# Kernel tuning notes

Hardware: AMD Instinct MI355X
Metric: run time of the kernel (lower is better)

## Reference

```python
import jax, jax.numpy as jnp
import numpy as np

SEQ_LEN = 256
SPIKE_STEPS = 7
BATCH = 128
IN_DIM = 96
HIDDEN = 512
OUT_DIM = 2
NLAYERS = 3
ALPHA = 2.0  # atan surrogate alpha = 2 * grad_slope


@jax.custom_vjp
def spike(x):
    # Heaviside fire with snntorch ATan surrogate gradient.
    return (x > 0).astype(x.dtype)


def _spike_fwd(x):
    return (x > 0).astype(x.dtype), x


def _spike_bwd(x, g):
    return (g * (ALPHA / 2.0) / (1.0 + (jnp.pi / 2.0 * ALPHA * x) ** 2),)


spike.defvjp(_spike_fwd, _spike_bwd)


def setup_inputs() -> dict:
    key = jax.random.key(0)
    ks = jax.random.split(key, 5)
    x = jax.random.normal(ks[0], (SEQ_LEN, BATCH, IN_DIM), dtype=jnp.float32)
    def w(k, shape, fan_in):
        return jax.random.normal(k, shape, dtype=jnp.float32) / np.float32(np.sqrt(fan_in))
    W0 = w(ks[1], (HIDDEN, IN_DIM), IN_DIM)
    W1 = w(ks[2], (HIDDEN, HIDDEN), HIDDEN)
    W2 = w(ks[3], (HIDDEN, HIDDEN), HIDDEN)
    Wout = w(ks[4], (OUT_DIM, HIDDEN), HIDDEN)
    betas = jnp.full((NLAYERS,), 0.95, dtype=jnp.float32)  # learnable beta per LIF layer
    thrs = jnp.ones((NLAYERS,), dtype=jnp.float32)          # learnable threshold per LIF layer
    return dict(x=x, W0=W0, W1=W1, W2=W2, Wout=Wout, betas=betas, thrs=thrs)


def reference(x, W0, W1, W2, Wout, betas, thrs):
    """Seq2SeqSNN forward (eval mode: dropout is identity).

    Membrane / integrator state is reset only once at the start (i == 0 path
    of the torch forward), so the whole seq_len * spike_steps loop is a single
    recurrence of length T = SEQ_LEN * SPIKE_STEPS.
    LIF layer (snntorch Leaky, reset_mechanism='zero'):
        reset = stop_grad(heaviside(mem_prev - thr))
        mem   = (beta * mem_prev + cur) * (1 - reset)
        spk   = spike(mem - thr)
    Output layer (Integrator, reset 'none'): mem_out += Wout @ z; the decoded
    prediction per sequence step is the mean of mem_out over spike_steps.
    """
    Ws = (W0, W1, W2)
    x_rep = jnp.repeat(x, SPIKE_STEPS, axis=0)  # [T, B, F], same input for each inner spike step

    mems0 = tuple(jnp.zeros((BATCH, HIDDEN), dtype=x.dtype) for _ in range(NLAYERS))
    mem_out0 = jnp.zeros((BATCH, OUT_DIM), dtype=x.dtype)

    def step(carry, xt):
        mems, mem_out = carry
        z = xt
        new_mems = []
        for j in range(NLAYERS):
            cur = z @ Ws[j].T                                   # [B, H]
            reset = jax.lax.stop_gradient(spike(mems[j] - thrs[j]))
            mem = (betas[j] * mems[j] + cur) * (1.0 - reset)
            z = spike(mem - thrs[j])                            # binary spikes
            new_mems.append(mem)
        mem_out = mem_out + z @ Wout.T                           # integrator, no reset
        return (tuple(new_mems), mem_out), mem_out

    _, mem_out_seq = jax.lax.scan(step, (mems0, mem_out0), x_rep)  # [T, B, 2]
    # decoder='mean' over the spike_steps axis of each sequence step
    preds = mem_out_seq.reshape(SEQ_LEN, SPIKE_STEPS, BATCH, OUT_DIM).mean(axis=1)
    return preds  # [SEQ_LEN, BATCH, OUT_DIM]
```

## Files before the change

### kernel.cpp

```cpp
#include <hip/hip_runtime.h>

#define SEQ_LEN 256
#define SPIKE_STEPS 7
#define BATCH 128
#define IN_DIM 96
#define HIDDEN 512
#define OUT_DIM 2

#define W0T_OFF 0
#define W1T_OFF (IN_DIM * HIDDEN)
#define W2T_OFF (W1T_OFF + HIDDEN * HIDDEN)
#define CTR_BYTE_OFF ((size_t)(W2T_OFF + HIDDEN * HIDDEN) * sizeof(float))
#define ZBUF_BYTE_OFF (CTR_BYTE_OFF + 1024)

typedef float f32x4 __attribute__((ext_vector_type(4)));
typedef float f32x2 __attribute__((ext_vector_type(2)));

__global__ void transpose_kernel(const float* __restrict__ in, float* __restrict__ out,
                                 int rows, int cols) {
    int idx = blockIdx.x * blockDim.x + threadIdx.x;
    if (idx < rows * cols) {
        int r = idx / cols, c = idx - r * cols;
        out[c * rows + r] = in[idx];
    }
}

__device__ __forceinline__ void pkfma(f32x2& acc, float w, f32x2 m) {
    const f32x2 wv = {w, w};
    acc = __builtin_elementwise_fma(wv, m, acc);
}

__device__ __forceinline__ void union_sum7(const float* __restrict__ W,
                                           const int* __restrict__ act,
                                           const float (* __restrict__ fmp)[8],
                                           int npad, int tid,
                                           f32x2* __restrict__ acc) {
    if (npad <= 0) return;
    const float* Wt = W + tid;
    int rows[16];
    float wc[16];
    {
        const int4* av = reinterpret_cast<const int4*>(act);
        int4 a0 = av[0], a1 = av[1], a2 = av[2], a3 = av[3];
        rows[0]=a0.x; rows[1]=a0.y; rows[2]=a0.z; rows[3]=a0.w;
        rows[4]=a1.x; rows[5]=a1.y; rows[6]=a1.z; rows[7]=a1.w;
        rows[8]=a2.x; rows[9]=a2.y; rows[10]=a2.z; rows[11]=a2.w;
        rows[12]=a3.x; rows[13]=a3.y; rows[14]=a3.z; rows[15]=a3.w;
    }
    #pragma unroll
    for (int k = 0; k < 16; ++k) wc[k] = Wt[rows[k] * HIDDEN];

    for (int n = 16; n < npad; n += 16) {
        int nrows[16];
        float wn[16];
        {
            const int4* av = reinterpret_cast<const int4*>(act + n);
            int4 a0 = av[0], a1 = av[1], a2 = av[2], a3 = av[3];
            nrows[0]=a0.x; nrows[1]=a0.y; nrows[2]=a0.z; nrows[3]=a0.w;
            nrows[4]=a1.x; nrows[5]=a1.y; nrows[6]=a1.z; nrows[7]=a1.w;
            nrows[8]=a2.x; nrows[9]=a2.y; nrows[10]=a2.z; nrows[11]=a2.w;
            nrows[12]=a3.x; nrows[13]=a3.y; nrows[14]=a3.z; nrows[15]=a3.w;
        }
        #pragma unroll
        for (int k = 0; k < 16; ++k) wn[k] = Wt[nrows[k] * HIDDEN];

        const int base = n - 16;
        #pragma unroll
        for (int k = 0; k < 16; ++k) {
            f32x4 fa = *reinterpret_cast<const f32x4*>(&fmp[base + k][0]);
            f32x4 fb = *reinterpret_cast<const f32x4*>(&fmp[base + k][4]);
            pkfma(acc[0], wc[k], __builtin_shufflevector(fa, fa, 0, 1));
            pkfma(acc[1], wc[k], __builtin_shufflevector(fa, fa, 2, 3));
            pkfma(acc[2], wc[k], __builtin_shufflevector(fb, fb, 0, 1));
            pkfma(acc[3], wc[k], __builtin_shufflevector(fb, fb, 2, 3));
        }
        #pragma unroll
        for (int k = 0; k < 16; ++k) wc[k] = wn[k];
    }
    const int base = npad - 16;
    #pragma unroll
    for (int k = 0; k < 16; ++k) {
        f32x4 fa = *reinterpret_cast<const f32x4*>(&fmp[base + k][0]);
        f32x4 fb = *reinterpret_cast<const f32x4*>(&fmp[base + k][4]);
        pkfma(acc[0], wc[k], __builtin_shufflevector(fa, fa, 0, 1));
        pkfma(acc[1], wc[k], __builtin_shufflevector(fa, fa, 2, 3));
        pkfma(acc[2], wc[k], __builtin_shufflevector(fb, fb, 0, 1));
        pkfma(acc[3], wc[k], __builtin_shufflevector(fb, fb, 2, 3));
    }
}

__device__ __forceinline__ int build_union(const unsigned long long (*zm7)[8],
                                           int* act, float (*fmp)[8],
                                           int wid, int lane, int tid, int m7) {
    unsigned long long um[8];
    #pragma unroll
    for (int q = 0; q < 8; ++q) {
        unsigned long long u = zm7[0][q];
        #pragma unroll
        for (int s = 1; s < SPIKE_STEPS; ++s) u |= zm7[s][q];
        um[q] = u;
    }
    int pre = 0, total = 0;
    #pragma unroll
    for (int q = 0; q < 8; ++q) {
        int p = __popcll(um[q]);
        total += p;
        if (q < wid) pre += p;
    }
    if (m7 != 0) {
        int rank = pre + __popcll(um[wid] & ((1ull << lane) - 1ull));
        act[rank] = tid;
        f32x4 v0, v4;
        #pragma unroll
        for (int s = 0; s < 4; ++s) v0[s] = ((m7 >> s) & 1) ? 1.0f : 0.0f;
        #pragma unroll
        for (int s = 0; s < 3; ++s) v4[s] = ((m7 >> (4 + s)) & 1) ? 1.0f : 0.0f;
        v4[3] = 0.f;
        *reinterpret_cast<f32x4*>(&fmp[rank][0]) = v0;
        *reinterpret_cast<f32x4*>(&fmp[rank][4]) = v4;
    }
    int npad = (total + 15) & ~15;
    if (tid < npad - total) {
        act[total + tid] = 0;
        const f32x4 z = {0.f, 0.f, 0.f, 0.f};
        *reinterpret_cast<f32x4*>(&fmp[total + tid][0]) = z;
        *reinterpret_cast<f32x4*>(&fmp[total + tid][4]) = z;
    }
    return npad;
}

__launch_bounds__(512, 1)
__global__ void snn_pipe_kernel(const float* __restrict__ x,
                                const float* __restrict__ Wout,
                                const float* __restrict__ betas,
                                const float* __restrict__ thrs,
                                const float* __restrict__ W0T,
                                const float* __restrict__ W1T,
                                const float* __restrict__ W2T,
                                unsigned long long* __restrict__ zbuf,
                                int* __restrict__ ctr,
                                float* __restrict__ out)
{
    const int b    = blockIdx.x >> 1;
    const int role = blockIdx.x & 1;
    const int tid  = threadIdx.x;
    const int lane = tid & 63;
    const int wid  = tid >> 6;

    __shared__ float xs[2][IN_DIM];
    __shared__ unsigned long long zm7[SPIKE_STEPS][8];
    __shared__ int act[HIDDEN];
    __shared__ __align__(16) float fmp[HIDDEN][8];
    __shared__ float red[16];

    if (role == 0) {
        const float beta0 = betas[0], beta1 = betas[1];
        const float thr0  = thrs[0],  thr1  = thrs[1];
        float mem0 = 0.f, mem1 = 0.f;
        unsigned long long* zb = zbuf + (size_t)b * SEQ_LEN * 56;

        if (tid < IN_DIM) xs[0][tid] = x[(0 * BATCH + b) * IN_DIM + tid];
        __syncthreads();

        for (int i = 0; i < SEQ_LEN; ++i) {
            const int cur = i & 1;

            float cur0 = 0.f;
            #pragma unroll 8
            for (int k = 0; k < IN_DIM; ++k)
                cur0 = __fmaf_rn(xs[cur][k], W0T[k * HIDDEN + tid], cur0);

            if (i + 1 < SEQ_LEN && tid < IN_DIM)
                xs[cur ^ 1][tid] = x[((i + 1) * BATCH + b) * IN_DIM + tid];

            int m7 = 0;
            #pragma unroll
            for (int s = 0; s < SPIKE_STEPS; ++s) {
                bool reset0 = (mem0 - thr0) > 0.f;
                mem0 = reset0 ? 0.f : __fadd_rn(__fmul_rn(beta0, mem0), cur0);
                bool z0 = (mem0 - thr0) > 0.f;
                m7 |= (int)z0 << s;
                unsigned long long bal = __ballot(z0);
                if (lane == 0) zm7[s][wid] = bal;
            }
            __syncthreads();

            int npad = build_union(zm7, act, fmp, wid, lane, tid, m7);
            __syncthreads();

            f32x2 acc[4] = {{0.f,0.f},{0.f,0.f},{0.f,0.f},{0.f,0.f}};
            union_sum7(W1T, act, fmp, npad, tid, acc);
            const float accs[SPIKE_STEPS] =
                {acc[0].x, acc[0].y, acc[1].x, acc[1].y, acc[2].x, acc[2].y, acc[3].x};

            #pragma unroll
            for (int s = 0; s < SPIKE_STEPS; ++s) {
                bool reset1 = (mem1 - thr1) > 0.f;
                mem1 = reset1 ? 0.f : __fadd_rn(__fmul_rn(beta1, mem1), accs[s]);
                bool z1 = (mem1 - thr1) > 0.f;
                unsigned long long bal1 = __ballot(z1);
                if (lane == 0)
                    __hip_atomic_store(&zb[(size_t)i * 56 + s * 8 + wid], bal1,
                                       __ATOMIC_RELAXED, __HIP_MEMORY_SCOPE_AGENT);
            }
            __syncthreads();
            if (tid == 0)
                __hip_atomic_store(&ctr[b], i + 1,
                                   __ATOMIC_RELAXED, __HIP_MEMORY_SCOPE_AGENT);
        }
    } else {
        const float beta2 = betas[2];
        const float thr2  = thrs[2];
        const float wo0 = Wout[tid];
        const float wo1 = Wout[HIDDEN + tid];
        float mem2 = 0.f;
        float a0s = 0.f, a1s = 0.f;
        const unsigned long long* zb = zbuf + (size_t)b * SEQ_LEN * 56;

        for (int i = 0; i < SEQ_LEN; ++i) {
            if (tid < 56) {
                while (__hip_atomic_load(&ctr[b], __ATOMIC_RELAXED,
                                         __HIP_MEMORY_SCOPE_AGENT) < i + 1)
                    __builtin_amdgcn_s_sleep(1);
                ((unsigned long long*)zm7)[tid] =
                    __hip_atomic_load(&zb[(size_t)i * 56 + tid],
                                      __ATOMIC_RELAXED, __HIP_MEMORY_SCOPE_AGENT);
            }
            __syncthreads();

            int m7 = 0;
            #pragma unroll
            for (int s = 0; s < SPIKE_STEPS; ++s)
                m7 |= (int)((zm7[s][wid] >> lane) & 1ull) << s;

            int npad = build_union(zm7, act, fmp, wid, lane, tid, m7);
            __syncthreads();

            f32x2 acc[4] = {{0.f,0.f},{0.f,0.f},{0.f,0.f},{0.f,0.f}};
            union_sum7(W2T, act, fmp, npad, tid, acc);
            const float accs[SPIKE_STEPS] =
                {acc[0].x, acc[0].y, acc[1].x, acc[1].y, acc[2].x, acc[2].y, acc[3].x};

            float w0 = 0.f, w1 = 0.f;
            #pragma unroll
            for (int s = 0; s < SPIKE_STEPS; ++s) {
                bool reset2 = (mem2 - thr2) > 0.f;
                mem2 = reset2 ? 0.f : __fadd_rn(__fmul_rn(beta2, mem2), accs[s]);
                bool z2 = (mem2 - thr2) > 0.f;
                a0s += z2 ? wo0 : 0.f;
                a1s += z2 ? wo1 : 0.f;
                w0 += a0s;
                w1 += a1s;
            }

            float r0 = w0, r1 = w1;
            #pragma unroll
            for (int off = 32; off > 0; off >>= 1) {
                r0 += __shfl_down(r0, off);
                r1 += __shfl_down(r1, off);
            }
            if (lane == 0) { red[wid * 2] = r0; red[wid * 2 + 1] = r1; }
            __syncthreads();
            if (tid == 0) {
                float s0 = 0.f, s1 = 0.f;
                #pragma unroll
                for (int q = 0; q < 8; ++q) { s0 += red[q * 2]; s1 += red[q * 2 + 1]; }
                out[(i * BATCH + b) * OUT_DIM + 0] = s0 / 7.0f;
                out[(i * BATCH + b) * OUT_DIM + 1] = s1 / 7.0f;
            }
        }
    }
}

extern "C" void kernel_launch(void* const* d_in, const int* in_sizes, int n_in,
                              void* d_out, int out_size, void* d_ws, size_t ws_size,
                              hipStream_t stream) {
    const float* x     = (const float*)d_in[0];
    const float* W0    = (const float*)d_in[1];
    const float* W1    = (const float*)d_in[2];
    const float* W2    = (const float*)d_in[3];
    const float* Wout  = (const float*)d_in[4];
    const float* betas = (const float*)d_in[5];
    const float* thrs  = (const float*)d_in[6];
    float* out = (float*)d_out;

    float* ws  = (float*)d_ws;
    float* W0T = ws + W0T_OFF;
    float* W1T = ws + W1T_OFF;
    float* W2T = ws + W2T_OFF;
    int* ctr = (int*)((char*)d_ws + CTR_BYTE_OFF);
    unsigned long long* zbuf = (unsigned long long*)((char*)d_ws + ZBUF_BYTE_OFF);

    {
        int n = HIDDEN * IN_DIM;
        transpose_kernel<<<(n + 255) / 256, 256, 0, stream>>>(W0, W0T, HIDDEN, IN_DIM);
    }
    {
        int n = HIDDEN * HIDDEN;
        transpose_kernel<<<(n + 255) / 256, 256, 0, stream>>>(W1, W1T, HIDDEN, HIDDEN);
        transpose_kernel<<<(n + 255) / 256, 256, 0, stream>>>(W2, W2T, HIDDEN, HIDDEN);
    }

    hipMemsetAsync((char*)d_ws + CTR_BYTE_OFF, 0, 1024, stream);

    snn_pipe_kernel<<<2 * BATCH, HIDDEN, 0, stream>>>(
        x, Wout, betas, thrs, W0T, W1T, W2T, zbuf, ctr, out);
}
```

Measured before the change: 2.946 ms.

## Merge producer/consumer blocks into one 1024-thread block with LDS handoff

Replaces the two-block-per-batch pipeline, which handed layer-1 spikes to layer 2 through global memory and an atomic counter spin-wait, with a single 1024-thread block per batch element. The first half computes layers 0-1 while the second half computes layer 2 for the previous step, exchanging spike masks through double-buffered shared memory and block barriers. This removes global-memory polling latency and the memset, but couples both halves to the same barriers, so each step waits for the slower half, and it doubles LDS usage per block.

```diff
diff --git a/kernel.cpp b/kernel.cpp
--- a/kernel.cpp
+++ b/kernel.cpp
@@ -10,8 +10,6 @@
 #define W0T_OFF 0
 #define W1T_OFF (IN_DIM * HIDDEN)
 #define W2T_OFF (W1T_OFF + HIDDEN * HIDDEN)
-#define CTR_BYTE_OFF ((size_t)(W2T_OFF + HIDDEN * HIDDEN) * sizeof(float))
-#define ZBUF_BYTE_OFF (CTR_BYTE_OFF + 1024)
 
 typedef float f32x4 __attribute__((ext_vector_type(4)));
 typedef float f32x2 __attribute__((ext_vector_type(2)));
@@ -33,10 +31,10 @@
 __device__ __forceinline__ void union_sum7(const float* __restrict__ W,
                                            const int* __restrict__ act,
                                            const float (* __restrict__ fmp)[8],
-                                           int npad, int tid,
+                                           int npad, int col,
                                            f32x2* __restrict__ acc) {
     if (npad <= 0) return;
-    const float* Wt = W + tid;
+    const float* Wt = W + col;
     int rows[16];
     float wc[16];
     {
@@ -89,15 +87,15 @@
     }
 }
 
-__device__ __forceinline__ int build_union(const unsigned long long (*zm7)[8],
+__device__ __forceinline__ int build_union(const unsigned long long (*zm)[8],
                                            int* act, float (*fmp)[8],
-                                           int wid, int lane, int tid, int m7) {
+                                           int hwid, int hlane, int htid, int m7) {
     unsigned long long um[8];
     #pragma unroll
     for (int q = 0; q < 8; ++q) {
-        unsigned long long u = zm7[0][q];
-        #pragma unroll
-        for (int s = 1; s < SPIKE_STEPS; ++s) u |= zm7[s][q];
+        unsigned long long u = zm[0][q];
+        #pragma unroll
+        for (int s = 1; s < SPIKE_STEPS; ++s) u |= zm[s][q];
         um[q] = u;
     }
     int pre = 0, total = 0;
@@ -105,11 +103,11 @@
     for (int q = 0; q < 8; ++q) {
         int p = __popcll(um[q]);
         total += p;
-        if (q < wid) pre += p;
+        if (q < hwid) pre += p;
     }
     if (m7 != 0) {
-        int rank = pre + __popcll(um[wid] & ((1ull << lane) - 1ull));
-        act[rank] = tid;
+        int rank = pre + __popcll(um[hwid] & ((1ull << hlane) - 1ull));
+        act[rank] = htid;
         f32x4 v0, v4;
         #pragma unroll
         for (int s = 0; s < 4; ++s) v0[s] = ((m7 >> s) & 1) ? 1.0f : 0.0f;
@@ -120,60 +118,65 @@
         *reinterpret_cast<f32x4*>(&fmp[rank][4]) = v4;
     }
     int npad = (total + 15) & ~15;
-    if (tid < npad - total) {
-        act[total + tid] = 0;
+    if (htid < npad - total) {
+        act[total + htid] = 0;
         const f32x4 z = {0.f, 0.f, 0.f, 0.f};
-        *reinterpret_cast<f32x4*>(&fmp[total + tid][0]) = z;
-        *reinterpret_cast<f32x4*>(&fmp[total + tid][4]) = z;
+        *reinterpret_cast<f32x4*>(&fmp[total + htid][0]) = z;
+        *reinterpret_cast<f32x4*>(&fmp[total + htid][4]) = z;
     }
     return npad;
 }
 
-__launch_bounds__(512, 1)
-__global__ void snn_pipe_kernel(const float* __restrict__ x,
-                                const float* __restrict__ Wout,
-                                const float* __restrict__ betas,
-                                const float* __restrict__ thrs,
-                                const float* __restrict__ W0T,
-                                const float* __restrict__ W1T,
-                                const float* __restrict__ W2T,
-                                unsigned long long* __restrict__ zbuf,
-                                int* __restrict__ ctr,
-                                float* __restrict__ out)
+__launch_bounds__(1024, 1)
+__global__ void snn_merged_kernel(const float* __restrict__ x,
+                                  const float* __restrict__ Wout,
+                                  const float* __restrict__ betas,
+                                  const float* __restrict__ thrs,
+                                  const float* __restrict__ W0T,
+                                  const float* __restrict__ W1T,
+                                  const float* __restrict__ W2T,
+                                  float* __restrict__ out)
 {
-    const int b    = blockIdx.x >> 1;
-    const int role = blockIdx.x & 1;
-    const int tid  = threadIdx.x;
-    const int lane = tid & 63;
-    const int wid  = tid >> 6;
+    const int b     = blockIdx.x;
+    const int tid   = threadIdx.x;
+    const int half  = tid >> 9;
+    const int htid  = tid & 511;
+    const int hlane = htid & 63;
+    const int hwid  = htid >> 6;
 
     __shared__ float xs[2][IN_DIM];
-    __shared__ unsigned long long zm7[SPIKE_STEPS][8];
-    __shared__ int act[HIDDEN];
-    __shared__ __align__(16) float fmp[HIDDEN][8];
+    __shared__ unsigned long long zm0[SPIKE_STEPS][8];
+    __shared__ unsigned long long zr[2][SPIKE_STEPS][8];
+    __shared__ int actF[HIDDEN];
+    __shared__ int actB[HIDDEN];
+    __shared__ __align__(16) float fmpF[HIDDEN][8];
+    __shared__ __align__(16) float fmpB[HIDDEN][8];
     __shared__ float red[16];
 
-    if (role == 0) {
-        const float beta0 = betas[0], beta1 = betas[1];
-        const float thr0  = thrs[0],  thr1  = thrs[1];
-        float mem0 = 0.f, mem1 = 0.f;
-        unsigned long long* zb = zbuf + (size_t)b * SEQ_LEN * 56;
-
-        if (tid < IN_DIM) xs[0][tid] = x[(0 * BATCH + b) * IN_DIM + tid];
-        __syncthreads();
-
-        for (int i = 0; i < SEQ_LEN; ++i) {
-            const int cur = i & 1;
-
+    float mem0 = 0.f, mem1 = 0.f;
+    float mem2 = 0.f, a0s = 0.f, a1s = 0.f;
+    const float beta0 = betas[0], beta1 = betas[1], beta2 = betas[2];
+    const float thr0  = thrs[0],  thr1  = thrs[1],  thr2  = thrs[2];
+    const float wo0 = Wout[htid];
+    const float wo1 = Wout[HIDDEN + htid];
+
+    if (half == 0 && tid < IN_DIM) xs[0][tid] = x[(0 * BATCH + b) * IN_DIM + tid];
+    __syncthreads();
+
+    for (int it = 0; it <= SEQ_LEN; ++it) {
+        const bool frun = (half == 0) && (it < SEQ_LEN);
+        const bool brun = (half == 1) && (it >= 1);
+
+        int m7 = 0;
+        if (frun) {
+            const int cur = it & 1;
             float cur0 = 0.f;
             #pragma unroll 8
             for (int k = 0; k < IN_DIM; ++k)
-                cur0 = __fmaf_rn(xs[cur][k], W0T[k * HIDDEN + tid], cur0);
-
-            if (i + 1 < SEQ_LEN && tid < IN_DIM)
-                xs[cur ^ 1][tid] = x[((i + 1) * BATCH + b) * IN_DIM + tid];
-
-            int m7 = 0;
+                cur0 = __fmaf_rn(xs[cur][k], W0T[k * HIDDEN + htid], cur0);
+            if (it + 1 < SEQ_LEN && htid < IN_DIM)
+                xs[cur ^ 1][htid] = x[((it + 1) * BATCH + b) * IN_DIM + htid];
+
             #pragma unroll
             for (int s = 0; s < SPIKE_STEPS; ++s) {
                 bool reset0 = (mem0 - thr0) > 0.f;
@@ -181,66 +184,39 @@
                 bool z0 = (mem0 - thr0) > 0.f;
                 m7 |= (int)z0 << s;
                 unsigned long long bal = __ballot(z0);
-                if (lane == 0) zm7[s][wid] = bal;
-            }
-            __syncthreads();
-
-            int npad = build_union(zm7, act, fmp, wid, lane, tid, m7);
-            __syncthreads();
-
+                if (hlane == 0) zm0[s][hwid] = bal;
+            }
+        } else if (brun) {
+            const unsigned long long (*zs)[8] = zr[(it - 1) & 1];
+            #pragma unroll
+            for (int s = 0; s < SPIKE_STEPS; ++s)
+                m7 |= (int)((zs[s][hwid] >> hlane) & 1ull) << s;
+        }
+        __syncthreads();
+
+        int npad = 0;
+        if (frun)      npad = build_union(zm0,              actF, fmpF, hwid, hlane, htid, m7);
+        else if (brun) npad = build_union(zr[(it - 1) & 1], actB, fmpB, hwid, hlane, htid, m7);
+        __syncthreads();
+
+        if (frun) {
             f32x2 acc[4] = {{0.f,0.f},{0.f,0.f},{0.f,0.f},{0.f,0.f}};
-            union_sum7(W1T, act, fmp, npad, tid, acc);
+            union_sum7(W1T, actF, fmpF, npad, htid, acc);
             const float accs[SPIKE_STEPS] =
                 {acc[0].x, acc[0].y, acc[1].x, acc[1].y, acc[2].x, acc[2].y, acc[3].x};
-
             #pragma unroll
             for (int s = 0; s < SPIKE_STEPS; ++s) {
                 bool reset1 = (mem1 - thr1) > 0.f;
                 mem1 = reset1 ? 0.f : __fadd_rn(__fmul_rn(beta1, mem1), accs[s]);
                 bool z1 = (mem1 - thr1) > 0.f;
                 unsigned long long bal1 = __ballot(z1);
-                if (lane == 0)
-                    __hip_atomic_store(&zb[(size_t)i * 56 + s * 8 + wid], bal1,
-                                       __ATOMIC_RELAXED, __HIP_MEMORY_SCOPE_AGENT);
-            }
-            __syncthreads();
-            if (tid == 0)
-                __hip_atomic_store(&ctr[b], i + 1,
-                                   __ATOMIC_RELAXED, __HIP_MEMORY_SCOPE_AGENT);
-        }
-    } else {
-        const float beta2 = betas[2];
-        const float thr2  = thrs[2];
-        const float wo0 = Wout[tid];
-        const float wo1 = Wout[HIDDEN + tid];
-        float mem2 = 0.f;
-        float a0s = 0.f, a1s = 0.f;
-        const unsigned long long* zb = zbuf + (size_t)b * SEQ_LEN * 56;
-
-        for (int i = 0; i < SEQ_LEN; ++i) {
-            if (tid < 56) {
-                while (__hip_atomic_load(&ctr[b], __ATOMIC_RELAXED,
-                                         __HIP_MEMORY_SCOPE_AGENT) < i + 1)
-                    __builtin_amdgcn_s_sleep(1);
-                ((unsigned long long*)zm7)[tid] =
-                    __hip_atomic_load(&zb[(size_t)i * 56 + tid],
-                                      __ATOMIC_RELAXED, __HIP_MEMORY_SCOPE_AGENT);
-            }
-            __syncthreads();
-
-            int m7 = 0;
-            #pragma unroll
-            for (int s = 0; s < SPIKE_STEPS; ++s)
-                m7 |= (int)((zm7[s][wid] >> lane) & 1ull) << s;
-
-            int npad = build_union(zm7, act, fmp, wid, lane, tid, m7);
-            __syncthreads();
-
+                if (hlane == 0) zr[it & 1][s][hwid] = bal1;
+            }
+        } else if (brun) {
             f32x2 acc[4] = {{0.f,0.f},{0.f,0.f},{0.f,0.f},{0.f,0.f}};
-            union_sum7(W2T, act, fmp, npad, tid, acc);
+            union_sum7(W2T, actB, fmpB, npad, htid, acc);
             const float accs[SPIKE_STEPS] =
                 {acc[0].x, acc[0].y, acc[1].x, acc[1].y, acc[2].x, acc[2].y, acc[3].x};
-
             float w0 = 0.f, w1 = 0.f;
             #pragma unroll
             for (int s = 0; s < SPIKE_STEPS; ++s) {
@@ -252,22 +228,22 @@
                 w0 += a0s;
                 w1 += a1s;
             }
-
             float r0 = w0, r1 = w1;
             #pragma unroll
             for (int off = 32; off > 0; off >>= 1) {
                 r0 += __shfl_down(r0, off);
                 r1 += __shfl_down(r1, off);
             }
-            if (lane == 0) { red[wid * 2] = r0; red[wid * 2 + 1] = r1; }
-            __syncthreads();
-            if (tid == 0) {
-                float s0 = 0.f, s1 = 0.f;
-                #pragma unroll
-                for (int q = 0; q < 8; ++q) { s0 += red[q * 2]; s1 += red[q * 2 + 1]; }
-                out[(i * BATCH + b) * OUT_DIM + 0] = s0 / 7.0f;
-                out[(i * BATCH + b) * OUT_DIM + 1] = s1 / 7.0f;
-            }
+            if (hlane == 0) { red[hwid * 2] = r0; red[hwid * 2 + 1] = r1; }
+        }
+        __syncthreads();
+
+        if (brun && htid == 0) {
+            float s0 = 0.f, s1 = 0.f;
+            #pragma unroll
+            for (int q = 0; q < 8; ++q) { s0 += red[q * 2]; s1 += red[q * 2 + 1]; }
+            out[((it - 1) * BATCH + b) * OUT_DIM + 0] = s0 / 7.0f;
+            out[((it - 1) * BATCH + b) * OUT_DIM + 1] = s1 / 7.0f;
         }
     }
 }
@@ -288,8 +264,6 @@
     float* W0T = ws + W0T_OFF;
     float* W1T = ws + W1T_OFF;
     float* W2T = ws + W2T_OFF;
-    int* ctr = (int*)((char*)d_ws + CTR_BYTE_OFF);
-    unsigned long long* zbuf = (unsigned long long*)((char*)d_ws + ZBUF_BYTE_OFF);
 
     {
         int n = HIDDEN * IN_DIM;
@@ -301,8 +275,6 @@
         transpose_kernel<<<(n + 255) / 256, 256, 0, stream>>>(W2, W2T, HIDDEN, HIDDEN);
     }
 
-    hipMemsetAsync((char*)d_ws + CTR_BYTE_OFF, 0, 1024, stream);
-
-    snn_pipe_kernel<<<2 * BATCH, HIDDEN, 0, stream>>>(
-        x, Wout, betas, thrs, W0T, W1T, W2T, zbuf, ctr, out);
-}
+    snn_merged_kernel<<<BATCH, 1024, 0, stream>>>(
+        x, Wout, betas, thrs, W0T, W1T, W2T, out);
+}
```

After: 4.270 ms. 44.9% more time.
